# Optimization experiments

Measured on AMD Instinct MI355X. Metric: run time of the kernel, lower is better.

Reference implementation:

```python
import jax, jax.numpy as jnp
import numpy as np

B, N, N_IN, MSG_HID, MSG_OUT, N_HID, N_OUT, K = 32, 128, 16, 64, 64, 64, 16, 4
E = N * (N - 1)  # 16256 directed edges, fully connected w/o self-loops


def setup_inputs() -> dict:
    key = jax.random.key(0)
    ks = jax.random.split(key, 8)
    # one-hot relation matrices (NRI convention)
    rows, cols = np.where(np.ones((N, N)) - np.eye(N))
    eye = np.eye(N, dtype=np.float32)
    rel_rec = jnp.asarray(eye[rows])   # [E, N]
    rel_send = jnp.asarray(eye[cols])  # [E, N]
    s = 0.1  # weight init scale
    return {
        "inputs": jax.random.normal(ks[0], (B, N_IN, N), jnp.float32),
        "rel_rec": rel_rec,
        "rel_send": rel_send,
        "rel_types": jax.nn.softmax(jax.random.normal(ks[1], (B, E, K), jnp.float32), axis=-1),
        "W1": jax.random.normal(ks[2], (K, 2 * N_IN, MSG_HID), jnp.float32) * s,
        "b1": jnp.zeros((K, MSG_HID), jnp.float32),
        "W2": jax.random.normal(ks[3], (K, MSG_HID, MSG_OUT), jnp.float32) * s,
        "b2": jnp.zeros((K, MSG_OUT), jnp.float32),
        "Wo1": jax.random.normal(ks[4], (MSG_OUT + N_IN, N_HID), jnp.float32) * s,
        "bo1": jnp.zeros((N_HID,), jnp.float32),
        "Wo2": jax.random.normal(ks[5], (N_HID, N_HID), jnp.float32) * s,
        "bo2": jnp.zeros((N_HID,), jnp.float32),
        "Wo3": jax.random.normal(ks[6], (N_HID, N_OUT), jnp.float32) * s,
        "bo3": jnp.zeros((N_OUT,), jnp.float32),
    }


def reference(inputs, rel_rec, rel_send, rel_types, W1, b1, W2, b2, Wo1, bo1, Wo2, bo2, Wo3, bo3):
    x = jnp.transpose(inputs, (0, 2, 1))                     # [B, N, n_in]
    senders = jnp.einsum('en,bnf->bef', rel_send, x)          # [B, E, n_in]
    receivers = jnp.einsum('en,bnf->bef', rel_rec, x)         # [B, E, n_in]
    pre_msg = jnp.concatenate([senders, receivers], axis=-1)  # [B, E, 2*n_in]
    all_msgs = jnp.zeros((pre_msg.shape[0], pre_msg.shape[1], W2.shape[-1]), pre_msg.dtype)
    for k in range(W1.shape[0]):  # small fixed loop over edge types
        m = jax.nn.relu(pre_msg @ W1[k] + b1[k])
        m = jax.nn.relu(m @ W2[k] + b2[k])
        all_msgs = all_msgs + m * rel_types[:, :, k:k + 1]
    # edge2node aggregation (no normalization in forward path, matches source)
    agg_msgs = jnp.einsum('bem,en->bnm', all_msgs, rel_rec)   # [B, N, msg_out]
    aug_msgs = jnp.concatenate([x, agg_msgs], axis=-1)        # [B, N, n_in+msg_out]
    h = jax.nn.relu(aug_msgs @ Wo1 + bo1)  # dropout disabled (eval mode)
    h = jax.nn.relu(h @ Wo2 + bo2)
    pred = h @ Wo3 + bo3                                      # [B, N, n_out]
    return jnp.transpose(pred, (0, 2, 1))                     # [B, n_out, N]
```

## Files before the change

kernel.cpp:

```cpp
#include <hip/hip_runtime.h>
#include <stdint.h>

#define B_  32
#define N_  128
#define NIN 16
#define K_  4
#define E_  (N_*(N_-1))

typedef float    f4 __attribute__((ext_vector_type(4)));
typedef _Float16 h8 __attribute__((ext_vector_type(8)));
typedef _Float16 h4 __attribute__((ext_vector_type(4)));

__global__ __launch_bounds__(256) void prep(
    const float* __restrict__ inp, const float* __restrict__ W1,
    const float* __restrict__ b1,  const float* __restrict__ W2,
    const float* __restrict__ rt,
    _Float16* __restrict__ Sh, _Float16* __restrict__ Rh,
    _Float16* __restrict__ w2h, _Float16* __restrict__ rtn)
{
    const int bid = blockIdx.x;
    const int tid = threadIdx.x;
    if (bid < 4096) {
        int gid = bid*256 + tid;
        int c = gid & 63;
        int n = (gid >> 6) & 127;
        int b = (gid >> 13) & 31;
        int k = gid >> 18;
        float s = 0.f, r = 0.f;
        const float* w1s = W1 + (k*32)*64 + c;
        const float* w1r = W1 + (k*32 + 16)*64 + c;
        const float* xp  = inp + (b*NIN)*N_ + n;
        #pragma unroll
        for (int f = 0; f < 16; ++f) {
            float xv = xp[f*N_];
            s += xv * w1s[f*64];
            r += xv * w1r[f*64];
        }
        r += b1[k*64 + c];
        Sh[gid] = (_Float16)s;
        Rh[gid] = (_Float16)r;
    } else if (bid < 4160) {
        int t = (bid - 4096)*256 + tid;
        int i    = t & 7;
        int lane = (t >> 3) & 63;
        int nt   = (t >> 9) & 3;
        int ks   = (t >> 11) & 1;
        int k    = t >> 12;
        int c = ks*32 + (lane >> 4)*8 + i;
        int o = nt*16 + (lane & 15);
        w2h[t] = (_Float16)W2[(k*64 + c)*64 + o];
    } else {
        int t = (bid - 4160)*256 + tid;
        int jg = t & 31;
        int r  = (t >> 5) & 127;
        int b  = t >> 12;
        const f4* rt4p = (const f4*)(rt + (size_t)(b*E_ + r*127)*4);
        #pragma unroll
        for (int u = 0; u < 4; ++u) {
            int j = jg*4 + u;
            if (j < 127) {
                f4 v = rt4p[j];
                int s = j + (j >= r ? 1 : 0);
                #pragma unroll
                for (int k = 0; k < 4; ++k)
                    rtn[((k*B_ + b)*N_ + r)*N_ + s] = (_Float16)v[k];
            } else {
                #pragma unroll
                for (int k = 0; k < 4; ++k)
                    rtn[((k*B_ + b)*N_ + r)*N_ + r] = (_Float16)0.f;
            }
        }
    }
}

__global__ __launch_bounds__(512) void edge_mfma(
    const _Float16* __restrict__ Sh, const _Float16* __restrict__ Rh,
    const _Float16* __restrict__ w2h, const _Float16* __restrict__ rtn,
    const float* __restrict__ b2, float* __restrict__ aggK)
{
    __shared__ _Float16 Ssw[N_*64];

    const int tid  = threadIdx.x;
    const int wave = tid >> 6;
    const int lane = tid & 63;
    const int col  = lane & 15;
    const int q    = lane >> 4;
    const int bid  = blockIdx.x;
    const int rt4  = bid & 3;
    const int b    = (bid >> 2) & 31;
    const int k    = bid >> 7;
    const int kb   = k*B_ + b;

    const _Float16* Sg = Sh + (size_t)kb*(N_*64);
    #pragma unroll
    for (int rnd = 0; rnd < 2; ++rnd) {
        int p  = rnd*512 + tid;
        int s  = p >> 3;
        int c8 = (p & 7) ^ (s & 7);
        h8 v = *(const h8*)(Sg + (s*8 + c8)*8);
        *(h8*)(Ssw + p*8) = v;
    }

    const h8* w2v = (const h8*)w2h;
    h8 w2f[2][4];
    #pragma unroll
    for (int ks = 0; ks < 2; ++ks)
        #pragma unroll
        for (int nt = 0; nt < 4; ++nt)
            w2f[ks][nt] = w2v[((k*2 + ks)*4 + nt)*64 + lane];

    f4 b2i[4];
    #pragma unroll
    for (int nt = 0; nt < 4; ++nt) {
        float v = b2[k*64 + nt*16 + col];
        b2i[nt][0] = v; b2i[nt][1] = v; b2i[nt][2] = v; b2i[nt][3] = v;
    }

    __syncthreads();

    const h8* Rv = (const h8*)Rh;
    const _Float16* rtbase = rtn + (size_t)kb*(N_*N_);
    const h8 zero8 = {0,0,0,0,0,0,0,0};

    #pragma unroll 1
    for (int rg = 0; rg < 4; ++rg) {
        const int r = rt4*32 + wave*4 + rg;
        h8 rf0 = Rv[(kb*N_ + r)*8 + q];
        h8 rf1 = Rv[(kb*N_ + r)*8 + 4 + q];
        const h4* rtp = (const h4*)(rtbase + r*N_);
        h4 rth[8];
        #pragma unroll
        for (int mt = 0; mt < 8; ++mt) rth[mt] = rtp[mt*4 + q];

        float aggacc[4] = {0.f, 0.f, 0.f, 0.f};
        #pragma unroll
        for (int mt = 0; mt < 8; ++mt) {
            int s  = mt*16 + col;
            int x0 = (s*8 + (q       ^ (s & 7)))*8;
            int x1 = (s*8 + ((4 + q) ^ (s & 7)))*8;
            h8 a0 = *(const h8*)(Ssw + x0);
            h8 a1 = *(const h8*)(Ssw + x1);
            a0 = __builtin_elementwise_max(a0 + rf0, zero8);
            a1 = __builtin_elementwise_max(a1 + rf1, zero8);
            float rtv[4];
            #pragma unroll
            for (int i = 0; i < 4; ++i) rtv[i] = (float)rth[mt][i];

            #pragma unroll
            for (int nt = 0; nt < 4; ++nt) {
                f4 acc = __builtin_amdgcn_mfma_f32_16x16x32_f16(a0, w2f[0][nt], b2i[nt], 0, 0, 0);
                acc     = __builtin_amdgcn_mfma_f32_16x16x32_f16(a1, w2f[1][nt], acc,    0, 0, 0);
                #pragma unroll
                for (int i = 0; i < 4; ++i)
                    aggacc[nt] += rtv[i] * fmaxf(acc[i], 0.f);
            }
        }
        #pragma unroll
        for (int nt = 0; nt < 4; ++nt) {
            float v = aggacc[nt];
            v += __shfl_xor(v, 16, 64);
            v += __shfl_xor(v, 32, 64);
            if (lane < 16) aggK[((size_t)kb*N_ + r)*64 + nt*16 + lane] = v;
        }
    }
}

__global__ __launch_bounds__(256) void node_mlp(
    const float* __restrict__ aggK, const float* __restrict__ inp,
    const float* __restrict__ Wo1, const float* __restrict__ bo1,
    const float* __restrict__ Wo2, const float* __restrict__ bo2,
    const float* __restrict__ Wo3, const float* __restrict__ bo3,
    float* __restrict__ out)
{
    __shared__ float W1s[80*64];
    __shared__ float W2s[64*64];
    __shared__ float W3s[64*16];
    __shared__ float bs[144];
    __shared__ float augs[4][2][80];
    __shared__ float h1s[4][2][64];
    __shared__ float h2s[4][2][64];

    const int tid  = threadIdx.x;
    const int wave = tid >> 6;
    const int lane = tid & 63;

    for (int i = tid; i < 80*64; i += 256) W1s[i] = Wo1[i];
    for (int i = tid; i < 64*64; i += 256) W2s[i] = Wo2[i];
    for (int i = tid; i < 64*16; i += 256) W3s[i] = Wo3[i];
    if (tid < 64)  bs[tid] = bo1[tid];
    else if (tid < 128) bs[tid] = bo2[tid - 64];
    else if (tid < 144) bs[tid] = bo3[tid - 128];
    __syncthreads();

    #pragma unroll
    for (int t = 0; t < 2; ++t) {
        const int node = blockIdx.x*8 + wave*2 + t;
        const int b = node >> 7, r = node & 127;
        if (lane < 16) augs[wave][t][lane] = inp[(b*NIN + lane)*N_ + r];
        float a = 0.f;
        #pragma unroll
        for (int k = 0; k < 4; ++k)
            a += aggK[(((size_t)k*B_ + b)*N_ + r)*64 + lane];
        augs[wave][t][16 + lane] = a;

        float s = bs[lane];
        #pragma unroll 8
        for (int i = 0; i < 80; ++i) s += augs[wave][t][i] * W1s[i*64 + lane];
        h1s[wave][t][lane] = fmaxf(s, 0.f);

        s = bs[64 + lane];
        #pragma unroll 8
        for (int i = 0; i < 64; ++i) s += h1s[wave][t][i] * W2s[i*64 + lane];
        h2s[wave][t][lane] = fmaxf(s, 0.f);

        if (lane < 16) {
            s = bs[128 + lane];
            #pragma unroll 8
            for (int i = 0; i < 64; ++i) s += h2s[wave][t][i] * W3s[i*16 + lane];
            out[(b*NIN + lane)*N_ + r] = s;
        }
    }
}

extern "C" void kernel_launch(void* const* d_in, const int* in_sizes, int n_in,
                              void* d_out, int out_size, void* d_ws, size_t ws_size,
                              hipStream_t stream)
{
    const float* inp = (const float*)d_in[0];
    const float* rt  = (const float*)d_in[3];
    const float* W1  = (const float*)d_in[4];
    const float* b1  = (const float*)d_in[5];
    const float* W2  = (const float*)d_in[6];
    const float* b2  = (const float*)d_in[7];
    const float* Wo1 = (const float*)d_in[8];
    const float* bo1 = (const float*)d_in[9];
    const float* Wo2 = (const float*)d_in[10];
    const float* bo2 = (const float*)d_in[11];
    const float* Wo3 = (const float*)d_in[12];
    const float* bo3 = (const float*)d_in[13];

    _Float16* Sh   = (_Float16*)d_ws;
    _Float16* Rh   = Sh + (1u << 20);
    _Float16* w2h  = Rh + (1u << 20);
    _Float16* rtn  = w2h + 16384;
    float*    aggK = (float*)(rtn + (1u << 21));

    hipLaunchKernelGGL(prep, dim3(4672), dim3(256), 0, stream,
                       inp, W1, b1, W2, rt, Sh, Rh, w2h, rtn);
    hipLaunchKernelGGL(edge_mfma, dim3(512), dim3(512), 0, stream,
                       Sh, Rh, w2h, rtn, b2, aggK);
    hipLaunchKernelGGL(node_mlp, dim3(512), dim3(256), 0, stream,
                       aggK, inp, Wo1, bo1, Wo2, bo2, Wo3, bo3, (float*)d_out);
}
```

Measured before the change: 140.5 us.

## Read rel_types directly in edge kernel, vectorize prep, use MFMA for node MLP

The prep kernel no longer builds a transposed fp16 copy of rel_types. The edge kernel now reads the fp32 rel_types with strided per-k loads, skipping the diagonal on the fly. The S/R projection in prep is vectorized to four channels per thread, and prep also converts the node-MLP weights to fp16 MFMA fragment layout. The node MLP is rewritten as an MFMA kernel over 64-node tiles with swizzled LDS. The aim is to remove the large rtn write/read pass and the scalar node MLP, at the cost of uncoalesced stride-4 rel_types loads in the edge loop, fewer blocks (64) in the node kernel, and fp16 rounding of activations.

```diff
diff --git a/kernel.cpp b/kernel.cpp
--- a/kernel.cpp
+++ b/kernel.cpp
@@ -14,33 +14,38 @@
 __global__ __launch_bounds__(256) void prep(
     const float* __restrict__ inp, const float* __restrict__ W1,
     const float* __restrict__ b1,  const float* __restrict__ W2,
-    const float* __restrict__ rt,
+    const float* __restrict__ Wo1, const float* __restrict__ Wo2,
+    const float* __restrict__ Wo3,
     _Float16* __restrict__ Sh, _Float16* __restrict__ Rh,
-    _Float16* __restrict__ w2h, _Float16* __restrict__ rtn)
+    _Float16* __restrict__ w2h, _Float16* __restrict__ wn)
 {
     const int bid = blockIdx.x;
     const int tid = threadIdx.x;
-    if (bid < 4096) {
+    if (bid < 1024) {
         int gid = bid*256 + tid;
-        int c = gid & 63;
-        int n = (gid >> 6) & 127;
-        int b = (gid >> 13) & 31;
-        int k = gid >> 18;
-        float s = 0.f, r = 0.f;
-        const float* w1s = W1 + (k*32)*64 + c;
-        const float* w1r = W1 + (k*32 + 16)*64 + c;
+        int c0 = (gid & 15)*4;
+        int n  = (gid >> 4) & 127;
+        int b  = (gid >> 11) & 31;
+        int k  = gid >> 16;
+        f4 s = {0.f,0.f,0.f,0.f};
+        f4 r = *(const f4*)(b1 + k*64 + c0);
         const float* xp  = inp + (b*NIN)*N_ + n;
+        const f4* w1s = (const f4*)(W1 + (k*32)*64 + c0);
+        const f4* w1r = (const f4*)(W1 + (k*32 + 16)*64 + c0);
         #pragma unroll
         for (int f = 0; f < 16; ++f) {
             float xv = xp[f*N_];
-            s += xv * w1s[f*64];
-            r += xv * w1r[f*64];
-        }
-        r += b1[k*64 + c];
-        Sh[gid] = (_Float16)s;
-        Rh[gid] = (_Float16)r;
-    } else if (bid < 4160) {
-        int t = (bid - 4096)*256 + tid;
+            s += xv * w1s[f*16];
+            r += xv * w1r[f*16];
+        }
+        int base = ((k*B_ + b)*N_ + n)*64 + c0;
+        h4 sh, rh;
+        #pragma unroll
+        for (int u = 0; u < 4; ++u) { sh[u] = (_Float16)s[u]; rh[u] = (_Float16)r[u]; }
+        *(h4*)(Sh + base) = sh;
+        *(h4*)(Rh + base) = rh;
+    } else if (bid < 1088) {
+        int t = (bid - 1024)*256 + tid;
         int i    = t & 7;
         int lane = (t >> 3) & 63;
         int nt   = (t >> 9) & 3;
@@ -50,32 +55,29 @@
         int o = nt*16 + (lane & 15);
         w2h[t] = (_Float16)W2[(k*64 + c)*64 + o];
     } else {
-        int t = (bid - 4160)*256 + tid;
-        int jg = t & 31;
-        int r  = (t >> 5) & 127;
-        int b  = t >> 12;
-        const f4* rt4p = (const f4*)(rt + (size_t)(b*E_ + r*127)*4);
-        #pragma unroll
-        for (int u = 0; u < 4; ++u) {
-            int j = jg*4 + u;
-            if (j < 127) {
-                f4 v = rt4p[j];
-                int s = j + (j >= r ? 1 : 0);
-                #pragma unroll
-                for (int k = 0; k < 4; ++k)
-                    rtn[((k*B_ + b)*N_ + r)*N_ + s] = (_Float16)v[k];
-            } else {
-                #pragma unroll
-                for (int k = 0; k < 4; ++k)
-                    rtn[((k*B_ + b)*N_ + r)*N_ + r] = (_Float16)0.f;
-            }
-        }
+        int t = (bid - 1088)*256 + tid;
+        int j    = t & 7;
+        int lane = (t >> 3) & 63;
+        int f    = t >> 9;
+        int col = lane & 15, q = lane >> 4, row = q*8 + j;
+        float v;
+        if (f < 12) {
+            int ks = f >> 2, nt = f & 3, i = ks*32 + row;
+            v = (i < 80) ? Wo1[i*64 + nt*16 + col] : 0.f;
+        } else if (f < 20) {
+            int g = f - 12, ks = g >> 2, nt = g & 3, i = ks*32 + row;
+            v = Wo2[i*64 + nt*16 + col];
+        } else {
+            int ks = f - 20, i = ks*32 + row;
+            v = Wo3[i*16 + col];
+        }
+        wn[t] = (_Float16)v;
     }
 }
 
 __global__ __launch_bounds__(512) void edge_mfma(
     const _Float16* __restrict__ Sh, const _Float16* __restrict__ Rh,
-    const _Float16* __restrict__ w2h, const _Float16* __restrict__ rtn,
+    const _Float16* __restrict__ w2h, const float* __restrict__ rt,
     const float* __restrict__ b2, float* __restrict__ aggK)
 {
     __shared__ _Float16 Ssw[N_*64];
@@ -119,7 +121,6 @@
     __syncthreads();
 
     const h8* Rv = (const h8*)Rh;
-    const _Float16* rtbase = rtn + (size_t)kb*(N_*N_);
     const h8 zero8 = {0,0,0,0,0,0,0,0};
 
     #pragma unroll 1
@@ -127,14 +128,19 @@
         const int r = rt4*32 + wave*4 + rg;
         h8 rf0 = Rv[(kb*N_ + r)*8 + q];
         h8 rf1 = Rv[(kb*N_ + r)*8 + 4 + q];
-        const h4* rtp = (const h4*)(rtbase + r*N_);
-        h4 rth[8];
-        #pragma unroll
-        for (int mt = 0; mt < 8; ++mt) rth[mt] = rtp[mt*4 + q];
+        const float* rtb = rt + ((size_t)(b*E_ + r*127))*4 + k;
 
         float aggacc[4] = {0.f, 0.f, 0.f, 0.f};
         #pragma unroll
         for (int mt = 0; mt < 8; ++mt) {
+            float rtv[4];
+            #pragma unroll
+            for (int i = 0; i < 4; ++i) {
+                int sdx = mt*16 + q*4 + i;
+                float v = 0.f;
+                if (sdx != r) v = rtb[(sdx - (sdx > r ? 1 : 0))*4];
+                rtv[i] = v;
+            }
             int s  = mt*16 + col;
             int x0 = (s*8 + (q       ^ (s & 7)))*8;
             int x1 = (s*8 + ((4 + q) ^ (s & 7)))*8;
@@ -142,9 +148,6 @@
             h8 a1 = *(const h8*)(Ssw + x1);
             a0 = __builtin_elementwise_max(a0 + rf0, zero8);
             a1 = __builtin_elementwise_max(a1 + rf1, zero8);
-            float rtv[4];
-            #pragma unroll
-            for (int i = 0; i < 4; ++i) rtv[i] = (float)rth[mt][i];
 
             #pragma unroll
             for (int nt = 0; nt < 4; ++nt) {
@@ -165,60 +168,120 @@
     }
 }
 
-__global__ __launch_bounds__(256) void node_mlp(
+__global__ __launch_bounds__(256) void node_mfma(
     const float* __restrict__ aggK, const float* __restrict__ inp,
-    const float* __restrict__ Wo1, const float* __restrict__ bo1,
-    const float* __restrict__ Wo2, const float* __restrict__ bo2,
-    const float* __restrict__ Wo3, const float* __restrict__ bo3,
-    float* __restrict__ out)
+    const _Float16* __restrict__ wn,
+    const float* __restrict__ bo1, const float* __restrict__ bo2,
+    const float* __restrict__ bo3, float* __restrict__ out)
 {
-    __shared__ float W1s[80*64];
-    __shared__ float W2s[64*64];
-    __shared__ float W3s[64*16];
-    __shared__ float bs[144];
-    __shared__ float augs[4][2][80];
-    __shared__ float h1s[4][2][64];
-    __shared__ float h2s[4][2][64];
-
-    const int tid  = threadIdx.x;
-    const int wave = tid >> 6;
-    const int lane = tid & 63;
-
-    for (int i = tid; i < 80*64; i += 256) W1s[i] = Wo1[i];
-    for (int i = tid; i < 64*64; i += 256) W2s[i] = Wo2[i];
-    for (int i = tid; i < 64*16; i += 256) W3s[i] = Wo3[i];
-    if (tid < 64)  bs[tid] = bo1[tid];
-    else if (tid < 128) bs[tid] = bo2[tid - 64];
-    else if (tid < 144) bs[tid] = bo3[tid - 128];
+    __shared__ _Float16 augH[64*128];
+    __shared__ _Float16 h12[64*64];
+
+    const int tid = threadIdx.x;
+    const int b   = blockIdx.x >> 1;
+    const int r0  = (blockIdx.x & 1)*64;
+
+    {
+        const int nl = tid >> 2, c4 = tid & 3;
+        const int r  = r0 + nl;
+        float xv[4];
+        #pragma unroll
+        for (int u = 0; u < 4; ++u)
+            xv[u] = inp[(b*NIN + c4*4 + u)*N_ + r];
+        f4 av[4];
+        #pragma unroll
+        for (int w = 0; w < 4; ++w) {
+            int c = w*16 + c4*4;
+            f4 a = {0.f,0.f,0.f,0.f};
+            #pragma unroll
+            for (int k = 0; k < 4; ++k)
+                a += *(const f4*)(aggK + (((size_t)k*B_ + b)*N_ + r)*64 + c);
+            av[w] = a;
+        }
+        #pragma unroll
+        for (int u = 0; u < 4; ++u) {
+            int i = c4*4 + u;
+            augH[nl*128 + (((i>>3) ^ (nl&15))<<3) + (i&7)] = (_Float16)xv[u];
+        }
+        #pragma unroll
+        for (int w = 0; w < 4; ++w)
+            #pragma unroll
+            for (int u = 0; u < 4; ++u) {
+                int i = 16 + w*16 + c4*4 + u;
+                augH[nl*128 + (((i>>3) ^ (nl&15))<<3) + (i&7)] = (_Float16)av[w][u];
+            }
+        if (c4 < 2)
+            #pragma unroll
+            for (int u = 0; u < 8; ++u) {
+                int i = 80 + c4*8 + u;
+                augH[nl*128 + (((i>>3) ^ (nl&15))<<3) + (i&7)] = (_Float16)0.f;
+            }
+    }
     __syncthreads();
 
-    #pragma unroll
-    for (int t = 0; t < 2; ++t) {
-        const int node = blockIdx.x*8 + wave*2 + t;
-        const int b = node >> 7, r = node & 127;
-        if (lane < 16) augs[wave][t][lane] = inp[(b*NIN + lane)*N_ + r];
-        float a = 0.f;
-        #pragma unroll
-        for (int k = 0; k < 4; ++k)
-            a += aggK[(((size_t)k*B_ + b)*N_ + r)*64 + lane];
-        augs[wave][t][16 + lane] = a;
-
-        float s = bs[lane];
-        #pragma unroll 8
-        for (int i = 0; i < 80; ++i) s += augs[wave][t][i] * W1s[i*64 + lane];
-        h1s[wave][t][lane] = fmaxf(s, 0.f);
-
-        s = bs[64 + lane];
-        #pragma unroll 8
-        for (int i = 0; i < 64; ++i) s += h1s[wave][t][i] * W2s[i*64 + lane];
-        h2s[wave][t][lane] = fmaxf(s, 0.f);
-
-        if (lane < 16) {
-            s = bs[128 + lane];
-            #pragma unroll 8
-            for (int i = 0; i < 64; ++i) s += h2s[wave][t][i] * W3s[i*16 + lane];
-            out[(b*NIN + lane)*N_ + r] = s;
-        }
+    const int mt  = tid >> 6, lane = tid & 63;
+    const int col = lane & 15, q = lane >> 4;
+    const h8* wv   = (const h8*)wn;
+    const h8* augV = (const h8*)augH;
+    const h8* hv   = (const h8*)h12;
+    const int nl   = mt*16 + col;
+
+    f4 acc[4];
+    #pragma unroll
+    for (int nt = 0; nt < 4; ++nt) {
+        float v = bo1[nt*16 + col];
+        acc[nt][0] = v; acc[nt][1] = v; acc[nt][2] = v; acc[nt][3] = v;
+    }
+    #pragma unroll
+    for (int ks = 0; ks < 3; ++ks) {
+        h8 af = augV[nl*16 + ((ks*4 + q) ^ col)];
+        #pragma unroll
+        for (int nt = 0; nt < 4; ++nt)
+            acc[nt] = __builtin_amdgcn_mfma_f32_16x16x32_f16(af, wv[(ks*4 + nt)*64 + lane], acc[nt], 0, 0, 0);
+    }
+    #pragma unroll
+    for (int nt = 0; nt < 4; ++nt)
+        #pragma unroll
+        for (int i = 0; i < 4; ++i) {
+            int n2 = mt*16 + q*4 + i, o = nt*16 + col;
+            h12[n2*64 + (((o>>3) ^ (n2&7))<<3) + (o&7)] = (_Float16)fmaxf(acc[nt][i], 0.f);
+        }
+
+    f4 acc2[4];
+    #pragma unroll
+    for (int nt = 0; nt < 4; ++nt) {
+        float v = bo2[nt*16 + col];
+        acc2[nt][0] = v; acc2[nt][1] = v; acc2[nt][2] = v; acc2[nt][3] = v;
+    }
+    #pragma unroll
+    for (int ks = 0; ks < 2; ++ks) {
+        h8 af = hv[nl*8 + ((ks*4 + q) ^ (col & 7))];
+        #pragma unroll
+        for (int nt = 0; nt < 4; ++nt)
+            acc2[nt] = __builtin_amdgcn_mfma_f32_16x16x32_f16(af, wv[(12 + ks*4 + nt)*64 + lane], acc2[nt], 0, 0, 0);
+    }
+    #pragma unroll
+    for (int nt = 0; nt < 4; ++nt)
+        #pragma unroll
+        for (int i = 0; i < 4; ++i) {
+            int n2 = mt*16 + q*4 + i, o = nt*16 + col;
+            h12[n2*64 + (((o>>3) ^ (n2&7))<<3) + (o&7)] = (_Float16)fmaxf(acc2[nt][i], 0.f);
+        }
+
+    f4 acc3;
+    {
+        float v = bo3[col];
+        acc3[0] = v; acc3[1] = v; acc3[2] = v; acc3[3] = v;
+    }
+    #pragma unroll
+    for (int ks = 0; ks < 2; ++ks) {
+        h8 af = hv[nl*8 + ((ks*4 + q) ^ (col & 7))];
+        acc3 = __builtin_amdgcn_mfma_f32_16x16x32_f16(af, wv[(20 + ks)*64 + lane], acc3, 0, 0, 0);
+    }
+    #pragma unroll
+    for (int i = 0; i < 4; ++i) {
+        int r = r0 + mt*16 + q*4 + i;
+        out[(b*NIN + col)*N_ + r] = acc3[i];
     }
 }
 
@@ -242,13 +305,13 @@
     _Float16* Sh   = (_Float16*)d_ws;
     _Float16* Rh   = Sh + (1u << 20);
     _Float16* w2h  = Rh + (1u << 20);
-    _Float16* rtn  = w2h + 16384;
-    float*    aggK = (float*)(rtn + (1u << 21));
-
-    hipLaunchKernelGGL(prep, dim3(4672), dim3(256), 0, stream,
-                       inp, W1, b1, W2, rt, Sh, Rh, w2h, rtn);
+    _Float16* wn   = w2h + 16384;
+    float*    aggK = (float*)(wn + 11264);
+
+    hipLaunchKernelGGL(prep, dim3(1132), dim3(256), 0, stream,
+                       inp, W1, b1, W2, Wo1, Wo2, Wo3, Sh, Rh, w2h, wn);
     hipLaunchKernelGGL(edge_mfma, dim3(512), dim3(512), 0, stream,
-                       Sh, Rh, w2h, rtn, b2, aggK);
-    hipLaunchKernelGGL(node_mlp, dim3(512), dim3(256), 0, stream,
-                       aggK, inp, Wo1, bo1, Wo2, bo2, Wo3, bo3, (float*)d_out);
+                       Sh, Rh, w2h, rt, b2, aggK);
+    hipLaunchKernelGGL(node_mfma, dim3(64), dim3(256), 0, stream,
+                       aggK, inp, wn, bo1, bo2, bo3, (float*)d_out);
 }
```

Result: slower. 143.6 us (+2.2%).
